# Optimization experiments

Hardware: AMD Instinct MI355X
Metric: run time of the kernel (lower is better)

## Reference

```python
import jax, jax.numpy as jnp
import numpy as np

H = 12        # num_attention_heads
A = 16        # agent_num
C = 768       # hidden_size


def setup_inputs() -> dict:
    key = jax.random.key(0)
    ks = jax.random.split(key, 16)
    B, N = 8, 4096
    std = 0.02
    return {
        "s1_hidden_states": jax.random.normal(ks[0], (B, N, C), jnp.float32),
        "s2_hidden_states": jax.random.normal(ks[1], (B, N, C), jnp.float32),
        "Wq": jax.random.normal(ks[2], (C, C), jnp.float32) * std,
        "bq": jnp.zeros((C,), jnp.float32),
        "Wk": jax.random.normal(ks[3], (C, C), jnp.float32) * std,
        "bk": jnp.zeros((C,), jnp.float32),
        "Wv": jax.random.normal(ks[4], (C, C), jnp.float32) * std,
        "bv": jnp.zeros((C,), jnp.float32),
        "an_bias": jax.random.normal(ks[5], (H, A, 7, 7), jnp.float32) * std,
        "na_bias": jax.random.normal(ks[6], (H, A, 7, 7), jnp.float32) * std,
        "ah_bias": jax.random.normal(ks[7], (1, H, A, A, 1), jnp.float32) * std,
        "aw_bias": jax.random.normal(ks[8], (1, H, A, 1, A), jnp.float32) * std,
        "ha_bias": jax.random.normal(ks[9], (1, H, A, 1, A), jnp.float32) * std,
        "wa_bias": jax.random.normal(ks[10], (1, H, 1, A, A), jnp.float32) * std,
    }


def reference(s1_hidden_states, s2_hidden_states, Wq, bq, Wk, bk, Wv, bv,
              an_bias, na_bias, ah_bias, aw_bias, ha_bias, wa_bias):
    b, n, c = s1_hidden_states.shape
    m = s2_hidden_states.shape[1]
    hd = c // H
    scale = hd ** -0.5

    q = s1_hidden_states @ Wq.T + bq            # (b, n, c)
    k = s2_hidden_states @ Wk.T + bk            # (b, m, c)
    v = s2_hidden_states @ Wv.T + bv            # (b, m, c)

    # AdaptiveAvgPool1d(A) with n % A == 0 -> uniform chunk mean
    agent = q.reshape(b, A, n // A, c).mean(axis=2)  # (b, A, c)

    def heads(x):
        return x.reshape(b, -1, H, hd).transpose(0, 2, 1, 3)

    qh, kh, vh = heads(q), heads(k), heads(v)        # (b,H,·,hd)
    ah = heads(agent)                                # (b,H,A,hd)

    # stage 1: agent -> keys.  bias is constant per (h, a) row.
    pb1 = jax.image.resize(an_bias, (H, A, A, A), method='bilinear').reshape(1, H, A, A * A)
    pb2 = (ah_bias + aw_bias).reshape(1, H, A, A * A)
    pb = (pb1 + pb2).mean(axis=-1)                   # (1, H, A)
    agent_attn = jnp.einsum('bhad,bhmd->bham', ah * scale, kh) + pb[:, :, :, None]
    agent_attn = jax.nn.softmax(agent_attn, axis=-1)
    agent_v = jnp.einsum('bham,bhmd->bhad', agent_attn, vh)  # (b,H,A,hd)

    # stage 2: queries -> agents.
    ab1 = jax.image.resize(na_bias, (H, A, A, A), method='bilinear') \
            .reshape(1, H, A, A * A).transpose(0, 1, 3, 2)   # (1,H,A*A,A)
    ab2 = (ha_bias + wa_bias).reshape(1, H, A * A, A)
    ab = (ab1 + ab2).mean(axis=-2)                   # (1, H, A)
    q_attn = jnp.einsum('bhnd,bhad->bhna', qh * scale, ah) + ab[:, :, None, :]
    q_attn = jax.nn.softmax(q_attn, axis=-1)
    x = jnp.einsum('bhna,bhad->bhnd', q_attn, agent_v)  # (b,H,n,hd)
    return x.transpose(0, 2, 1, 3).reshape(b, n, c)
```

## Files before the change

kernel.cpp:

```cpp
#include <hip/hip_runtime.h>
#include <cstdint>
#include <cstddef>

typedef unsigned short ushort_t;
typedef unsigned int uint;

typedef __attribute__((ext_vector_type(8))) short short8;
typedef __attribute__((ext_vector_type(4))) float floatx4;

#define CDIM 768

__device__ __forceinline__ float bfu(ushort_t u) {
    return __uint_as_float(((uint)u) << 16);
}
__device__ __forceinline__ void bf2(uint u, float& lo, float& hi) {
    lo = __uint_as_float(u << 16);
    hi = __uint_as_float(u & 0xffff0000u);
}
__device__ __forceinline__ ushort_t f2bfu(float f) {
    uint u = __float_as_uint(f);
    u += 0x7fffu + ((u >> 16) & 1u);
    return (ushort_t)(u >> 16);
}
__device__ __forceinline__ uint pack2(float a, float b) {
    return (uint)f2bfu(a) | ((uint)f2bfu(b) << 16);
}
__device__ __forceinline__ uint cvt2(float lo, float hi) {
    uint r;
    asm("v_cvt_pk_bf16_f32 %0, %1, %2" : "=v"(r) : "v"(lo), "v"(hi));
    return r;
}
__device__ __forceinline__ void gload_lds16(const void* g, void* l) {
    __builtin_amdgcn_global_load_lds(
        (__attribute__((address_space(1))) void*)(uintptr_t)g,
        (__attribute__((address_space(3))) void*)l, 16, 0, 0);
}

__global__ __launch_bounds__(256) void cvt_w(
    const float* __restrict__ Wq, const float* __restrict__ Wk,
    const float* __restrict__ Wv, ushort_t* __restrict__ wb)
{
    const int m = blockIdx.y;
    const float* src = (m == 0) ? Wq : (m == 1 ? Wk : Wv);
    ushort_t* dst = wb + (size_t)m * 589824;
    const int i = (blockIdx.x * 256 + threadIdx.x) * 8;
    const float4 f0 = *(const float4*)(src + i);
    const float4 f1 = *(const float4*)(src + i + 4);
    uint4 u;
    u.x = pack2(f0.x, f0.y);
    u.y = pack2(f0.z, f0.w);
    u.z = pack2(f1.x, f1.y);
    u.w = pack2(f1.z, f1.w);
    *(uint4*)(dst + i) = u;
}

__global__ __launch_bounds__(256) void init_agent(const float* __restrict__ bq,
                                                  float* __restrict__ agent)
{
    const int bh = blockIdx.x;
    const int h = bh % 12;
    for (int i = threadIdx.x; i < 1024; i += 256)
        agent[(size_t)bh * 1024 + i] = bq[h * 64 + (i & 63)];
}

__global__ __launch_bounds__(256, 2) void gemm_qkv(
    const float* __restrict__ s1, const float* __restrict__ s2,
    const ushort_t* __restrict__ wb,
    const float* __restrict__ bq, const float* __restrict__ bk, const float* __restrict__ bv,
    ushort_t* __restrict__ qo, ushort_t* __restrict__ ko, ushort_t* __restrict__ vo,
    float* __restrict__ agent)
{
    const int z = blockIdx.z;
    const float* A        = (z == 0) ? s1 : s2;
    const ushort_t* W     = wb + (size_t)z * 589824;
    const float* bias     = (z == 0) ? bq : (z == 1 ? bk : bv);
    ushort_t* out         = (z == 0) ? qo : (z == 1 ? ko : vo);

    __shared__ ushort_t At[128 * 64];
    __shared__ ushort_t Wt[128 * 64];

    const int tid  = threadIdx.x;
    const int wave = tid >> 6;
    const int lane = tid & 63;
    const int wm = wave >> 1, wn = wave & 1;

    const int id   = blockIdx.x + (blockIdx.y << 8);
    const int id2  = (id & 7) * 192 + (id >> 3);
    const int row0 = (id2 / 6) * 128;
    const int col0 = (id2 % 6) * 128;

    const int sro = lane >> 3;
    const int sch = ((lane & 7) ^ sro) * 8;
    const float*    gaF = A + (size_t)(row0 + wave * 32 + sro) * CDIM + sch;
    const ushort_t* gwB = W + (size_t)(col0 + wave * 32 + sro) * CDIM + sch;

    floatx4 acc[4][4];
    #pragma unroll
    for (int i = 0; i < 4; ++i)
        #pragma unroll
        for (int j = 0; j < 4; ++j)
            acc[i][j] = (floatx4){0.f, 0.f, 0.f, 0.f};

    const int q4 = lane >> 4, r16 = lane & 15;

    float4 ra[4][2];
    #pragma unroll
    for (int i = 0; i < 4; ++i) {
        const float* p = gaF + (size_t)i * 8 * CDIM;
        ra[i][0] = *(const float4*)(p);
        ra[i][1] = *(const float4*)(p + 4);
    }

    for (int kt = 0; kt < CDIM; kt += 64) {
        __syncthreads();
        #pragma unroll
        for (int i = 0; i < 4; ++i)
            gload_lds16(gwB + (size_t)i * 8 * CDIM + kt, &Wt[(wave * 32 + i * 8) * 64]);
        #pragma unroll
        for (int i = 0; i < 4; ++i) {
            uint4 u;
            u.x = cvt2(ra[i][0].x, ra[i][0].y);
            u.y = cvt2(ra[i][0].z, ra[i][0].w);
            u.z = cvt2(ra[i][1].x, ra[i][1].y);
            u.w = cvt2(ra[i][1].z, ra[i][1].w);
            *(uint4*)&At[(wave * 32 + i * 8 + sro) * 64 + (lane & 7) * 8] = u;
        }
        __syncthreads();
        if (kt + 64 < CDIM) {
            #pragma unroll
            for (int i = 0; i < 4; ++i) {
                const float* p = gaF + (size_t)i * 8 * CDIM + kt + 64;
                ra[i][0] = *(const float4*)(p);
                ra[i][1] = *(const float4*)(p + 4);
            }
        }
        #pragma unroll
        for (int ks = 0; ks < 2; ++ks) {
            short8 af[4], bfr[4];
            #pragma unroll
            for (int mt = 0; mt < 4; ++mt) {
                const int row = wm * 64 + mt * 16 + r16;
                const int ch  = (ks * 4 + q4) ^ (row & 7);
                af[mt] = *(const short8*)&At[row * 64 + ch * 8];
            }
            #pragma unroll
            for (int nt = 0; nt < 4; ++nt) {
                const int row = wn * 64 + nt * 16 + r16;
                const int ch  = (ks * 4 + q4) ^ (row & 7);
                bfr[nt] = *(const short8*)&Wt[row * 64 + ch * 8];
            }
            #pragma unroll
            for (int mt = 0; mt < 4; ++mt)
                #pragma unroll
                for (int nt = 0; nt < 4; ++nt)
                    acc[mt][nt] = __builtin_amdgcn_mfma_f32_16x16x32_bf16(
                        af[mt], bfr[nt], acc[mt][nt], 0, 0, 0);
        }
    }

    const int b = row0 >> 12;
    const int m_base = row0 & 4095;
    #pragma unroll
    for (int nt = 0; nt < 4; ++nt) {
        const int col = col0 + wn * 64 + nt * 16 + r16;
        const int h = col >> 6, d = col & 63;
        const float bb = bias[col];
        ushort_t* ob = out + ((size_t)(b * 12 + h) * 4096) * 64 + d;
        float psum = 0.f;
        #pragma unroll
        for (int mt = 0; mt < 4; ++mt) {
            const int m = m_base + wm * 64 + mt * 16 + q4 * 4;
            #pragma unroll
            for (int r = 0; r < 4; ++r) {
                ob[(size_t)(m + r) * 64] = f2bfu(acc[mt][nt][r] + bb);
                psum += acc[mt][nt][r];
            }
        }
        if (z == 0) {
            psum += __shfl_xor(psum, 16);
            psum += __shfl_xor(psum, 32);
            if (q4 == 0)
                atomicAdd(&agent[(size_t)(b * 12 + h) * 1024 + (m_base >> 8) * 64 + d],
                          psum * (1.0f / 256.0f));
        }
    }
}

__global__ void bias_ab_k(const float* __restrict__ na, const float* __restrict__ ha,
                          const float* __restrict__ wa, float* __restrict__ ab)
{
    const int t = threadIdx.x;
    if (t >= 192) return;
    const int h = t >> 4, a = t & 15;
    const float cw[7] = {2.25f, 2.34375f, 2.28125f, 2.25f, 2.28125f, 2.34375f, 2.25f};
    float acc = 0.f;
    const float* nb = na + (h * 16 + a) * 49;
    for (int i = 0; i < 7; ++i)
        for (int j = 0; j < 7; ++j)
            acc += cw[i] * cw[j] * nb[i * 7 + j];
    acc *= (1.0f / 256.0f);
    float s = 0.f;
    for (int p = 0; p < 16; ++p)
        s += ha[(h * 16 + p) * 16 + a] + wa[(h * 16 + p) * 16 + a];
    ab[t] = acc + s * (1.0f / 16.0f);
}

__global__ __launch_bounds__(256) void stage1(
    const ushort_t* __restrict__ k_hm, const ushort_t* __restrict__ v_hm,
    const float* __restrict__ agent, float* __restrict__ Sp, float* __restrict__ avp)
{
    const int bh = blockIdx.x, z = blockIdx.y;
    const int tid = threadIdx.x;
    __shared__ float ahs[1024];
    __shared__ ushort_t E2[512 * 20];

    for (int i = tid; i < 1024; i += 256)
        ahs[i] = agent[(size_t)bh * 1024 + i] * 0.125f;
    __syncthreads();

    const int m0 = z * 512;
    const ushort_t* kb = k_hm + ((size_t)bh * 4096 + m0) * 64;

    {
        const uint4* krA = (const uint4*)(kb + (size_t)tid * 64);
        const uint4* krB = (const uint4*)(kb + (size_t)(tid + 256) * 64);
        uint kuA[16], kuB[16];
        #pragma unroll
        for (int i = 0; i < 4; ++i) {
            uint4 ua = krA[i], ub = krB[i];
            kuA[i*4+0] = ua.x; kuA[i*4+1] = ua.y; kuA[i*4+2] = ua.z; kuA[i*4+3] = ua.w;
            kuB[i*4+0] = ub.x; kuB[i*4+1] = ub.y; kuB[i*4+2] = ub.z; kuB[i*4+3] = ub.w;
        }
        float dsA[16], dsB[16];
        #pragma unroll
        for (int a = 0; a < 16; ++a) { dsA[a] = 0.f; dsB[a] = 0.f; }
        #pragma unroll
        for (int c = 0; c < 16; ++c) {
            float a0, a1, a2, a3, b0, b1, b2, b3;
            bf2(kuA[2*c],   a0, a1); bf2(kuA[2*c+1], a2, a3);
            bf2(kuB[2*c],   b0, b1); bf2(kuB[2*c+1], b2, b3);
            #pragma unroll
            for (int a = 0; a < 16; ++a) {
                const floatx4 av = *(const floatx4*)&ahs[a * 64 + c * 4];
                dsA[a] += a0 * av[0] + a1 * av[1] + a2 * av[2] + a3 * av[3];
                dsB[a] += b0 * av[0] + b1 * av[1] + b2 * av[2] + b3 * av[3];
            }
        }
        uint eA[8], eB[8];
        #pragma unroll
        for (int a2 = 0; a2 < 8; ++a2) {
            eA[a2] = pack2(__expf(dsA[2*a2]), __expf(dsA[2*a2+1]));
            eB[a2] = pack2(__expf(dsB[2*a2]), __expf(dsB[2*a2+1]));
        }
        uint2* dA = (uint2*)&E2[(size_t)tid * 20];
        uint2* dB = (uint2*)&E2[(size_t)(tid + 256) * 20];
        dA[0] = make_uint2(eA[0], eA[1]); dA[1] = make_uint2(eA[2], eA[3]);
        dA[2] = make_uint2(eA[4], eA[5]); dA[3] = make_uint2(eA[6], eA[7]);
        dB[0] = make_uint2(eB[0], eB[1]); dB[1] = make_uint2(eB[2], eB[3]);
        dB[2] = make_uint2(eB[4], eB[5]); dB[3] = make_uint2(eB[6], eB[7]);
    }
    __syncthreads();

    const int d = tid & 63, g = tid >> 6;
    const ushort_t* vb = v_hm + ((size_t)bh * 4096 + m0) * 64 + d;
    float acc0 = 0, acc1 = 0, acc2 = 0, acc3 = 0;
    float ss0 = 0, ss1 = 0, ss2 = 0, ss3 = 0;
    for (int ml = 0; ml < 512; ++ml) {
        const float vv = bfu(vb[(size_t)ml * 64]);
        const uint2 ee = *(const uint2*)&E2[(size_t)ml * 20 + g * 4];
        float e0, e1, e2, e3;
        bf2(ee.x, e0, e1);
        bf2(ee.y, e2, e3);
        acc0 += e0 * vv; ss0 += e0;
        acc1 += e1 * vv; ss1 += e1;
        acc2 += e2 * vv; ss2 += e2;
        acc3 += e3 * vv; ss3 += e3;
    }
    float* avz = avp + (size_t)(z * 96 + bh) * 1024;
    avz[(g * 4 + 0) * 64 + d] = acc0;
    avz[(g * 4 + 1) * 64 + d] = acc1;
    avz[(g * 4 + 2) * 64 + d] = acc2;
    avz[(g * 4 + 3) * 64 + d] = acc3;
    if (d == 0) {
        float* Sz = Sp + (z * 96 + bh) * 16;
        Sz[g * 4 + 0] = ss0;
        Sz[g * 4 + 1] = ss1;
        Sz[g * 4 + 2] = ss2;
        Sz[g * 4 + 3] = ss3;
    }
}

__global__ __launch_bounds__(256) void stage2(
    const ushort_t* __restrict__ q_hm, const float* __restrict__ avp,
    const float* __restrict__ Sp, const float* __restrict__ agent,
    const float* __restrict__ ab, float* __restrict__ out)
{
    const int nb = blockIdx.x, bh = blockIdx.y;
    const int b = bh / 12, h = bh % 12;
    const int tid = threadIdx.x;
    __shared__ float ahs[1024];
    __shared__ float avn[1024];
    __shared__ float abl[16];

    for (int i = tid; i < 1024; i += 256) {
        const int a = i >> 6;
        ahs[i] = agent[(size_t)bh * 1024 + i] * 0.125f;
        float num = 0.f, den = 0.f;
        #pragma unroll
        for (int zz = 0; zz < 8; ++zz) {
            num += avp[(size_t)(zz * 96 + bh) * 1024 + i];
            den += Sp[(zz * 96 + bh) * 16 + a];
        }
        avn[i] = num / den;
    }
    if (tid < 16) abl[tid] = ab[h * 16 + tid];
    __syncthreads();

    const int n0 = nb * 512;
    const uint4* qrA = (const uint4*)(q_hm + ((size_t)bh * 4096 + n0 + tid) * 64);
    const uint4* qrB = (const uint4*)(q_hm + ((size_t)bh * 4096 + n0 + tid + 256) * 64);
    uint quA[16], quB[16];
    #pragma unroll
    for (int i = 0; i < 4; ++i) {
        uint4 ua = qrA[i], ub = qrB[i];
        quA[i*4+0] = ua.x; quA[i*4+1] = ua.y; quA[i*4+2] = ua.z; quA[i*4+3] = ua.w;
        quB[i*4+0] = ub.x; quB[i*4+1] = ub.y; quB[i*4+2] = ub.z; quB[i*4+3] = ub.w;
    }
    float dsA[16], dsB[16];
    #pragma unroll
    for (int a = 0; a < 16; ++a) { float t = abl[a]; dsA[a] = t; dsB[a] = t; }
    #pragma unroll
    for (int c = 0; c < 16; ++c) {
        float a0, a1, a2, a3, b0, b1, b2, b3;
        bf2(quA[2*c],   a0, a1); bf2(quA[2*c+1], a2, a3);
        bf2(quB[2*c],   b0, b1); bf2(quB[2*c+1], b2, b3);
        #pragma unroll
        for (int a = 0; a < 16; ++a) {
            const floatx4 av = *(const floatx4*)&ahs[a * 64 + c * 4];
            dsA[a] += a0 * av[0] + a1 * av[1] + a2 * av[2] + a3 * av[3];
            dsB[a] += b0 * av[0] + b1 * av[1] + b2 * av[2] + b3 * av[3];
        }
    }
    float psA = 0.f, psB = 0.f;
    #pragma unroll
    for (int a = 0; a < 16; ++a) {
        dsA[a] = __expf(dsA[a]); psA += dsA[a];
        dsB[a] = __expf(dsB[a]); psB += dsB[a];
    }
    const float rA = 1.0f / psA, rB = 1.0f / psB;
    #pragma unroll
    for (int a = 0; a < 16; ++a) { dsA[a] *= rA; dsB[a] *= rB; }

    float* oA = out + ((size_t)b * 4096 + n0 + tid) * CDIM + h * 64;
    float* oB = oA + (size_t)256 * CDIM;
    #pragma unroll
    for (int dc = 0; dc < 16; ++dc) {
        floatx4 sA = {0.f, 0.f, 0.f, 0.f}, sB = {0.f, 0.f, 0.f, 0.f};
        #pragma unroll
        for (int a = 0; a < 16; ++a) {
            const floatx4 av = *(const floatx4*)&avn[a * 64 + dc * 4];
            sA += dsA[a] * av;
            sB += dsB[a] * av;
        }
        *(floatx4*)(oA + dc * 4) = sA;
        *(floatx4*)(oB + dc * 4) = sB;
    }
}

extern "C" void kernel_launch(void* const* d_in, const int* in_sizes, int n_in,
                              void* d_out, int out_size, void* d_ws, size_t ws_size,
                              hipStream_t stream) {
    (void)in_sizes; (void)n_in; (void)out_size; (void)ws_size;
    const float* s1 = (const float*)d_in[0];
    const float* s2 = (const float*)d_in[1];
    const float* Wq = (const float*)d_in[2];
    const float* bq = (const float*)d_in[3];
    const float* Wk = (const float*)d_in[4];
    const float* bk = (const float*)d_in[5];
    const float* Wv = (const float*)d_in[6];
    const float* bv = (const float*)d_in[7];
    const float* na = (const float*)d_in[9];
    const float* ha = (const float*)d_in[12];
    const float* wa = (const float*)d_in[13];
    float* out = (float*)d_out;

    char* ws = (char*)d_ws;
    ushort_t* q_hm = (ushort_t*)(ws);
    ushort_t* k_hm = (ushort_t*)(ws + 50331648);
    ushort_t* v_hm = (ushort_t*)(ws + 100663296);
    float* agent   = (float*)(ws + 150994944);
    float* Sp      = (float*)(ws + 151388160);
    float* avp     = (float*)(ws + 151437312);
    float* ab      = (float*)(ws + 154583040);
    ushort_t* wb   = (ushort_t*)(ws + 154583808);

    cvt_w      <<<dim3(288, 3),    256, 0, stream>>>(Wq, Wk, Wv, wb);
    init_agent <<<dim3(96),        256, 0, stream>>>(bq, agent);
    gemm_qkv   <<<dim3(256, 6, 3), 256, 0, stream>>>(s1, s2, wb, bq, bk, bv,
                                                     q_hm, k_hm, v_hm, agent);
    bias_ab_k  <<<1, 256, 0, stream>>>(na, ha, wa, ab);
    stage1     <<<dim3(96, 8),     256, 0, stream>>>(k_hm, v_hm, agent, Sp, avp);
    stage2     <<<dim3(8, 96),     256, 0, stream>>>(q_hm, avp, Sp, agent, ab, out);
}
```

Measured before the change: 324.4 us.

## Move stage2 score and output products onto bf16 MFMA with split-precision compensation

Stage2 now computes the query-agent scores and the probability-times-agent_v products with 16x16x32 bf16 MFMA instructions instead of scalar FMAs. To keep accuracy it splits agent and agent_v into a bf16 high part plus a bf16 residual and issues extra MFMAs for the residual terms. Softmax normalisation uses cross-lane shuffles, and the grid doubles to 16x96 with 64 rows per wave. The aim is to cut the VALU-bound compute of stage2. The costs are extra conversion and shuffle work, half-empty MFMA K-slots, and a small precision change from bf16 splitting.

```diff
diff --git a/kernel.cpp b/kernel.cpp
--- a/kernel.cpp
+++ b/kernel.cpp
@@ -29,6 +29,11 @@
     uint r;
     asm("v_cvt_pk_bf16_f32 %0, %1, %2" : "=v"(r) : "v"(lo), "v"(hi));
     return r;
+}
+__device__ __forceinline__ short8 mk8(uint a, uint b, uint c, uint d) {
+    union { uint4 u; short8 s; } x;
+    x.u = (uint4){a, b, c, d};
+    return x.s;
 }
 __device__ __forceinline__ void gload_lds16(const void* g, void* l) {
     __builtin_amdgcn_global_load_lds(
@@ -295,75 +300,121 @@
     const float* __restrict__ Sp, const float* __restrict__ agent,
     const float* __restrict__ ab, float* __restrict__ out)
 {
-    const int nb = blockIdx.x, bh = blockIdx.y;
+    const int nb = blockIdx.x;
+    const int bh = blockIdx.y;
     const int b = bh / 12, h = bh % 12;
     const int tid = threadIdx.x;
-    __shared__ float ahs[1024];
+    const int g = (tid >> 4) & 3;
+    const int t = tid & 15;
+    const int w = tid >> 6;
     __shared__ float avn[1024];
-    __shared__ float abl[16];
-
-    for (int i = tid; i < 1024; i += 256) {
-        const int a = i >> 6;
-        ahs[i] = agent[(size_t)bh * 1024 + i] * 0.125f;
-        float num = 0.f, den = 0.f;
+
+    {
+        const int i4 = tid * 4;
+        const int a = i4 >> 6;
+        floatx4 num = {0.f, 0.f, 0.f, 0.f};
+        float den = 0.f;
         #pragma unroll
         for (int zz = 0; zz < 8; ++zz) {
-            num += avp[(size_t)(zz * 96 + bh) * 1024 + i];
+            num += *(const floatx4*)&avp[(size_t)(zz * 96 + bh) * 1024 + i4];
             den += Sp[(zz * 96 + bh) * 16 + a];
         }
-        avn[i] = num / den;
-    }
-    if (tid < 16) abl[tid] = ab[h * 16 + tid];
+        const float r = 1.0f / den;
+        *(floatx4*)&avn[i4] = num * r;
+    }
     __syncthreads();
 
-    const int n0 = nb * 512;
-    const uint4* qrA = (const uint4*)(q_hm + ((size_t)bh * 4096 + n0 + tid) * 64);
-    const uint4* qrB = (const uint4*)(q_hm + ((size_t)bh * 4096 + n0 + tid + 256) * 64);
-    uint quA[16], quB[16];
-    #pragma unroll
-    for (int i = 0; i < 4; ++i) {
-        uint4 ua = qrA[i], ub = qrB[i];
-        quA[i*4+0] = ua.x; quA[i*4+1] = ua.y; quA[i*4+2] = ua.z; quA[i*4+3] = ua.w;
-        quB[i*4+0] = ub.x; quB[i*4+1] = ub.y; quB[i*4+2] = ub.z; quB[i*4+3] = ub.w;
-    }
-    float dsA[16], dsB[16];
-    #pragma unroll
-    for (int a = 0; a < 16; ++a) { float t = abl[a]; dsA[a] = t; dsB[a] = t; }
-    #pragma unroll
-    for (int c = 0; c < 16; ++c) {
-        float a0, a1, a2, a3, b0, b1, b2, b3;
-        bf2(quA[2*c],   a0, a1); bf2(quA[2*c+1], a2, a3);
-        bf2(quB[2*c],   b0, b1); bf2(quB[2*c+1], b2, b3);
-        #pragma unroll
-        for (int a = 0; a < 16; ++a) {
-            const floatx4 av = *(const floatx4*)&ahs[a * 64 + c * 4];
-            dsA[a] += a0 * av[0] + a1 * av[1] + a2 * av[2] + a3 * av[3];
-            dsB[a] += b0 * av[0] + b1 * av[1] + b2 * av[2] + b3 * av[3];
-        }
-    }
-    float psA = 0.f, psB = 0.f;
-    #pragma unroll
-    for (int a = 0; a < 16; ++a) {
-        dsA[a] = __expf(dsA[a]); psA += dsA[a];
-        dsB[a] = __expf(dsB[a]); psB += dsB[a];
-    }
-    const float rA = 1.0f / psA, rB = 1.0f / psB;
-    #pragma unroll
-    for (int a = 0; a < 16; ++a) { dsA[a] *= rA; dsB[a] *= rB; }
-
-    float* oA = out + ((size_t)b * 4096 + n0 + tid) * CDIM + h * 64;
-    float* oB = oA + (size_t)256 * CDIM;
-    #pragma unroll
-    for (int dc = 0; dc < 16; ++dc) {
-        floatx4 sA = {0.f, 0.f, 0.f, 0.f}, sB = {0.f, 0.f, 0.f, 0.f};
-        #pragma unroll
-        for (int a = 0; a < 16; ++a) {
-            const floatx4 av = *(const floatx4*)&avn[a * 64 + dc * 4];
-            sA += dsA[a] * av;
-            sB += dsB[a] * av;
-        }
-        *(floatx4*)(oA + dc * 4) = sA;
-        *(floatx4*)(oB + dc * 4) = sB;
+    short8 ahA[2], ahE[2];
+    #pragma unroll
+    for (int k0 = 0; k0 < 2; ++k0) {
+        const float* p = agent + (size_t)bh * 1024 + t * 64 + k0 * 32 + g * 8;
+        const float4 f0 = *(const float4*)p;
+        const float4 f1 = *(const float4*)(p + 4);
+        const float v[8] = {f0.x, f0.y, f0.z, f0.w, f1.x, f1.y, f1.z, f1.w};
+        uint u[4], e[4];
+        #pragma unroll
+        for (int j = 0; j < 4; ++j) {
+            const float a0 = v[2*j] * 0.125f, a1 = v[2*j+1] * 0.125f;
+            u[j] = cvt2(a0, a1);
+            float b0, b1; bf2(u[j], b0, b1);
+            e[j] = cvt2(a0 - b0, a1 - b1);
+        }
+        ahA[k0] = mk8(u[0], u[1], u[2], u[3]);
+        ahE[k0] = mk8(e[0], e[1], e[2], e[3]);
+    }
+
+    short8 avf[4], ave[4];
+    #pragma unroll
+    for (int dt = 0; dt < 4; ++dt) {
+        uint u[4] = {0, 0, 0, 0}, e[4] = {0, 0, 0, 0};
+        if (g < 2) {
+            #pragma unroll
+            for (int j = 0; j < 4; ++j) {
+                const float a0 = avn[(8*g + 2*j)     * 64 + dt * 16 + t];
+                const float a1 = avn[(8*g + 2*j + 1) * 64 + dt * 16 + t];
+                u[j] = cvt2(a0, a1);
+                float b0, b1; bf2(u[j], b0, b1);
+                e[j] = cvt2(a0 - b0, a1 - b1);
+            }
+        }
+        avf[dt] = mk8(u[0], u[1], u[2], u[3]);
+        ave[dt] = mk8(e[0], e[1], e[2], e[3]);
+    }
+
+    float abv[4];
+    #pragma unroll
+    for (int r = 0; r < 4; ++r) abv[r] = ab[h * 16 + 4 * g + r];
+
+    const int src0 = (t + 32 * g) & 63;
+    const int src1 = (src0 + 16) & 63;
+    const int n0 = nb * 256 + w * 64;
+    const ushort_t* qb = q_hm + ((size_t)bh * 4096 + n0) * 64;
+    float* ob = out + ((size_t)b * 4096 + n0) * CDIM + h * 64;
+
+    #pragma unroll
+    for (int ti = 0; ti < 4; ++ti) {
+        const ushort_t* qp = qb + (size_t)(ti * 16 + t) * 64 + g * 8;
+        const short8 qB0 = *(const short8*)(qp);
+        const short8 qB1 = *(const short8*)(qp + 32);
+
+        floatx4 sc = {0.f, 0.f, 0.f, 0.f};
+        sc = __builtin_amdgcn_mfma_f32_16x16x32_bf16(ahA[0], qB0, sc, 0, 0, 0);
+        sc = __builtin_amdgcn_mfma_f32_16x16x32_bf16(ahA[1], qB1, sc, 0, 0, 0);
+        sc = __builtin_amdgcn_mfma_f32_16x16x32_bf16(ahE[0], qB0, sc, 0, 0, 0);
+        sc = __builtin_amdgcn_mfma_f32_16x16x32_bf16(ahE[1], qB1, sc, 0, 0, 0);
+
+        const float e0 = __expf(sc[0] + abv[0]);
+        const float e1 = __expf(sc[1] + abv[1]);
+        const float e2 = __expf(sc[2] + abv[2]);
+        const float e3 = __expf(sc[3] + abv[3]);
+        float s = e0 + e1 + e2 + e3;
+        s += __shfl_xor(s, 16);
+        s += __shfl_xor(s, 32);
+        const float rs = 1.0f / s;
+        const float p0 = e0 * rs, p1 = e1 * rs, p2 = e2 * rs, p3 = e3 * rs;
+
+        const uint P0 = cvt2(p0, p1), P1 = cvt2(p2, p3);
+        float q0, q1, q2, q3;
+        bf2(P0, q0, q1); bf2(P1, q2, q3);
+        const uint E0 = cvt2(p0 - q0, p1 - q1), E1 = cvt2(p2 - q2, p3 - q3);
+
+        uint w0 = __shfl(P0, src0), w1 = __shfl(P1, src0);
+        uint w2 = __shfl(P0, src1), w3 = __shfl(P1, src1);
+        uint x0 = __shfl(E0, src0), x1 = __shfl(E1, src0);
+        uint x2 = __shfl(E0, src1), x3 = __shfl(E1, src1);
+        if (g >= 2) { w0 = w1 = w2 = w3 = 0; x0 = x1 = x2 = x3 = 0; }
+        const short8 pf = mk8(w0, w1, w2, w3);
+        const short8 pe = mk8(x0, x1, x2, x3);
+
+        float* op = ob + (size_t)(ti * 16 + t) * CDIM + 4 * g;
+        #pragma unroll
+        for (int dt = 0; dt < 4; ++dt) {
+            floatx4 od = {0.f, 0.f, 0.f, 0.f};
+            od = __builtin_amdgcn_mfma_f32_16x16x32_bf16(avf[dt], pf, od, 0, 0, 0);
+            od = __builtin_amdgcn_mfma_f32_16x16x32_bf16(avf[dt], pe, od, 0, 0, 0);
+            od = __builtin_amdgcn_mfma_f32_16x16x32_bf16(ave[dt], pf, od, 0, 0, 0);
+            *(floatx4*)(op + dt * 16) = od;
+        }
     }
 }
 
@@ -400,5 +451,5 @@
                                                      q_hm, k_hm, v_hm, agent);
     bias_ab_k  <<<1, 256, 0, stream>>>(na, ha, wa, ab);
     stage1     <<<dim3(96, 8),     256, 0, stream>>>(k_hm, v_hm, agent, Sp, avp);
-    stage2     <<<dim3(8, 96),     256, 0, stream>>>(q_hm, avp, Sp, agent, ab, out);
-}
+    stage2     <<<dim3(16, 96),    256, 0, stream>>>(q_hm, avp, Sp, agent, ab, out);
+}
```

Result: faster. 304.4 us (-6.2%).
